# Performance work log

Hardware: AMD Instinct MI355X
Metric: run time of the kernel (lower is better)

## Reference

```python
import jax, jax.numpy as jnp
import numpy as np

SZ = 3072
D = 1024
B, T = 4, 8192
VOCAB = 50257


def setup_inputs() -> dict:
    key = jax.random.key(0)
    k1, k2, k3 = jax.random.split(key, 3)
    t = jax.random.randint(k1, (B, T), 0, VOCAB, dtype=jnp.int32)
    tab = jax.random.normal(k2, (SZ, D), dtype=jnp.float32)
    w_proj = jax.random.normal(k3, (D, D), dtype=jnp.float32) / np.sqrt(D)
    return {"t": t, "tab": tab, "w_proj": w_proj}


def _hash_idx(t, sz):
    # prev token, padded with 0 at position 0
    prev = jnp.pad(t[:, :-1], ((0, 0), (1, 0)))
    # (t*31337 + prev*1000003) % sz, computed overflow-safely in int32
    # using modular arithmetic: (a*b) % m == ((a%m)*(b%m)) % m
    a = (t % sz) * (31337 % sz)
    b = (prev % sz) * (1000003 % sz)
    return (a + b) % sz


def reference(t, tab, w_proj):
    idx = _hash_idx(t, SZ)              # [B, T] in [0, SZ)
    emb = tab[idx]                      # [B, T, D] gather
    # F.linear(x, W) = x @ W.T
    return jnp.einsum('btd,ed->bte', emb, w_proj)
```

## Files before the change

kernel.cpp:

```cpp
#include <hip/hip_runtime.h>
#include <hip/hip_bf16.h>
#include <stdint.h>

#define SZ 3072
#define D_ 1024
#define BB 4
#define TT 8192
#define NROWS (BB * TT)

typedef unsigned short u16;
typedef __bf16 bf16x8 __attribute__((ext_vector_type(8)));
typedef float f32x4 __attribute__((ext_vector_type(4)));


__device__ __forceinline__ u16 f2bf(float f) {
    union { float f; uint32_t u; } c;
    c.f = f;
    uint32_t u = c.u;
    uint32_t r = (u + 0x7FFFu + ((u >> 16) & 1u)) >> 16;
    return (u16)r;
}

__device__ __forceinline__ void gload_lds16(const void* g, void* l) {
    __builtin_amdgcn_global_load_lds(
        (__attribute__((address_space(1))) void*)(void*)g,
        (__attribute__((address_space(3))) void*)l,
        16, 0, 0);
}

__device__ __forceinline__ int hash_pair(int cur, int prev) {
    int a = (cur % SZ) * (31337 % SZ);
    int b = (prev % SZ) * (1000003 % SZ);
    return (a + b) % SZ;
}


__global__ __launch_bounds__(256) void convert_kernel(
    const float* __restrict__ tab, const float* __restrict__ w,
    u16* __restrict__ tabb, u16* __restrict__ wb) {
    const int NT4 = SZ * D_ / 4;
    const int NTOT = NT4 + D_ * D_ / 4;
    int i = blockIdx.x * 256 + threadIdx.x;
    if (i >= NTOT) return;
    const float4* src;
    u16* dst;
    int o;
    if (i < NT4) { src = (const float4*)tab; dst = tabb; o = i; }
    else         { src = (const float4*)w;   dst = wb;   o = i - NT4; }
    float4 v = src[o];
    unsigned long long pack =
        (unsigned long long)f2bf(v.x) |
        ((unsigned long long)f2bf(v.y) << 16) |
        ((unsigned long long)f2bf(v.z) << 32) |
        ((unsigned long long)f2bf(v.w) << 48);
    *(unsigned long long*)&dst[o * 4] = pack;
}


__global__ __launch_bounds__(256) void hash_kernel(
    const int* __restrict__ t, int* __restrict__ idx) {
    int i = blockIdx.x * 256 + threadIdx.x;
    if (i >= NROWS) return;
    int j = i & (TT - 1);
    int cur = t[i];
    int prev = (j == 0) ? 0 : t[i - 1];
    idx[i] = hash_pair(cur, prev);
}


__global__ __launch_bounds__(256) void gemm_p_kernel(
    const u16* __restrict__ Ab,
    const u16* __restrict__ Wb,
    float* __restrict__ P) {
    __shared__ __align__(16) u16 As[128][32];
    __shared__ __align__(16) u16 Ws[128][32];

    const int tid = threadIdx.x;
    const int brow = blockIdx.x >> 3;
    const int bcol = blockIdx.x & 7;
    const int row0 = brow << 7;
    const int col0 = bcol << 7;
    const int lane = tid & 63;
    const int w = tid >> 6;
    const int wr = (w >> 1) << 6;
    const int wc = (w & 1) << 6;
    const int lrow = lane & 15;
    const int k8 = (lane >> 4) << 3;

    const int c0 = tid, c1 = tid + 256;
    const int r0 = c0 >> 2, kk0 = (c0 & 3) << 3;
    const int r1 = c1 >> 2, kk1 = (c1 & 3) << 3;

    f32x4 acc[4][4];
#pragma unroll
    for (int m = 0; m < 4; ++m)
#pragma unroll
        for (int n = 0; n < 4; ++n)
            acc[m][n] = f32x4{0.f, 0.f, 0.f, 0.f};

    for (int k0 = 0; k0 < D_; k0 += 32) {
        gload_lds16(&Ab[(row0 + r0) * D_ + k0 + kk0], &As[r0][kk0]);
        gload_lds16(&Ab[(row0 + r1) * D_ + k0 + kk1], &As[r1][kk1]);
        gload_lds16(&Wb[(col0 + r0) * D_ + k0 + kk0], &Ws[r0][kk0]);
        gload_lds16(&Wb[(col0 + r1) * D_ + k0 + kk1], &Ws[r1][kk1]);
        __syncthreads();

        bf16x8 av[4], bv[4];
#pragma unroll
        for (int m = 0; m < 4; ++m)
            av[m] = *(const bf16x8*)&As[wr + m * 16 + lrow][k8];
#pragma unroll
        for (int n = 0; n < 4; ++n)
            bv[n] = *(const bf16x8*)&Ws[wc + n * 16 + lrow][k8];
#pragma unroll
        for (int m = 0; m < 4; ++m)
#pragma unroll
            for (int n = 0; n < 4; ++n)
                acc[m][n] = __builtin_amdgcn_mfma_f32_16x16x32_bf16(
                    av[m], bv[n], acc[m][n], 0, 0, 0);
        __syncthreads();
    }

    const int rbase = (lane >> 4) << 2;
#pragma unroll
    for (int m = 0; m < 4; ++m)
#pragma unroll
        for (int n = 0; n < 4; ++n)
#pragma unroll
            for (int r = 0; r < 4; ++r)
                P[(row0 + wr + m * 16 + rbase + r) * D_ + col0 + wc + n * 16 + lrow] =
                    acc[m][n][r];
}


__global__ __launch_bounds__(256) void gather_kernel(
    const float* __restrict__ P, const int* __restrict__ idx,
    float* __restrict__ out) {
    const int total = NROWS * (D_ / 4);
    const float4* P4 = (const float4*)P;
    float4* O4 = (float4*)out;
    for (int v = blockIdx.x * 256 + threadIdx.x; v < total; v += gridDim.x * 256) {
        int row = v >> 8;
        int c4 = v & 255;
        int s = idx[row];
        O4[v] = P4[s * 256 + c4];
    }
}


__global__ __launch_bounds__(256) void fallback_kernel(
    const int* __restrict__ t, const float* __restrict__ tab,
    const float* __restrict__ w, float* __restrict__ out) {
    __shared__ float emb[D_];
    int row = blockIdx.x;
    int j = row & (TT - 1);
    int cur = t[row];
    int prev = (j == 0) ? 0 : t[row - 1];
    int s = hash_pair(cur, prev);
    for (int d = threadIdx.x; d < D_; d += 256) emb[d] = tab[s * D_ + d];
    __syncthreads();
    for (int e = threadIdx.x; e < D_; e += 256) {
        float accv = 0.f;
        const float* wrow = &w[e * D_];
        for (int d = 0; d < D_; ++d) accv += emb[d] * wrow[d];
        out[(size_t)row * D_ + e] = accv;
    }
}


extern "C" void kernel_launch(void* const* d_in, const int* in_sizes, int n_in,
                              void* d_out, int out_size, void* d_ws, size_t ws_size,
                              hipStream_t stream) {
    const int* t = (const int*)d_in[0];
    const float* tab = (const float*)d_in[1];
    const float* w = (const float*)d_in[2];
    float* out = (float*)d_out;

    const size_t off_tabb = 0;
    const size_t off_wb   = (size_t)SZ * D_ * 2;
    const size_t off_P    = off_wb + (size_t)D_ * D_ * 2;
    const size_t off_idx  = off_P + (size_t)SZ * D_ * 4;
    const size_t need     = off_idx + (size_t)NROWS * 4;

    if (ws_size < need) {
        fallback_kernel<<<NROWS, 256, 0, stream>>>(t, tab, w, out);
        return;
    }

    u16* tabb = (u16*)((char*)d_ws + off_tabb);
    u16* wb   = (u16*)((char*)d_ws + off_wb);
    float* P  = (float*)((char*)d_ws + off_P);
    int* idx  = (int*)((char*)d_ws + off_idx);

    convert_kernel<<<4096, 256, 0, stream>>>(tab, w, tabb, wb);
    hash_kernel<<<NROWS / 256, 256, 0, stream>>>(t, idx);
    gemm_p_kernel<<<(SZ / 128) * (D_ / 128), 256, 0, stream>>>(tabb, wb, P);
    gather_kernel<<<2048, 256, 0, stream>>>(P, idx, out);
}
```

Before: 194.0 us.

## Fuse hash into gather, shrink GEMM tiles to 64x64 with XCD remap, nontemporal stores

Drops the separate hash kernel and its index buffer by recomputing the hash inside the gather kernel from the token array. The output is written with nontemporal stores so the large streaming output does not pollute cache. The projection GEMM tile shrinks from 128x128 to 64x64, giving four times as many workgroups, and block ids are remapped across the eight XCDs. The smaller tiles raise parallelism on a small GEMM but lower data reuse per workgroup.

```diff
diff --git a/kernel.cpp b/kernel.cpp
--- a/kernel.cpp
+++ b/kernel.cpp
@@ -57,65 +57,53 @@
 }
 
 
-__global__ __launch_bounds__(256) void hash_kernel(
-    const int* __restrict__ t, int* __restrict__ idx) {
-    int i = blockIdx.x * 256 + threadIdx.x;
-    if (i >= NROWS) return;
-    int j = i & (TT - 1);
-    int cur = t[i];
-    int prev = (j == 0) ? 0 : t[i - 1];
-    idx[i] = hash_pair(cur, prev);
-}
-
-
 __global__ __launch_bounds__(256) void gemm_p_kernel(
     const u16* __restrict__ Ab,
     const u16* __restrict__ Wb,
     float* __restrict__ P) {
-    __shared__ __align__(16) u16 As[128][32];
-    __shared__ __align__(16) u16 Ws[128][32];
+    __shared__ __align__(16) u16 As[64][32];
+    __shared__ __align__(16) u16 Ws[64][32];
+
+    const int bid = blockIdx.x;
+    const int wgid = (bid & 7) * 96 + (bid >> 3);
+    const int brow = wgid >> 4;
+    const int bcol = wgid & 15;
+    const int row0 = brow << 6;
+    const int col0 = bcol << 6;
 
     const int tid = threadIdx.x;
-    const int brow = blockIdx.x >> 3;
-    const int bcol = blockIdx.x & 7;
-    const int row0 = brow << 7;
-    const int col0 = bcol << 7;
     const int lane = tid & 63;
     const int w = tid >> 6;
-    const int wr = (w >> 1) << 6;
-    const int wc = (w & 1) << 6;
+    const int wr = (w >> 1) << 5;
+    const int wc = (w & 1) << 5;
     const int lrow = lane & 15;
     const int k8 = (lane >> 4) << 3;
 
-    const int c0 = tid, c1 = tid + 256;
-    const int r0 = c0 >> 2, kk0 = (c0 & 3) << 3;
-    const int r1 = c1 >> 2, kk1 = (c1 & 3) << 3;
+    const int r0 = tid >> 2, kk0 = (tid & 3) << 3;
 
-    f32x4 acc[4][4];
+    f32x4 acc[2][2];
 #pragma unroll
-    for (int m = 0; m < 4; ++m)
+    for (int m = 0; m < 2; ++m)
 #pragma unroll
-        for (int n = 0; n < 4; ++n)
+        for (int n = 0; n < 2; ++n)
             acc[m][n] = f32x4{0.f, 0.f, 0.f, 0.f};
 
     for (int k0 = 0; k0 < D_; k0 += 32) {
         gload_lds16(&Ab[(row0 + r0) * D_ + k0 + kk0], &As[r0][kk0]);
-        gload_lds16(&Ab[(row0 + r1) * D_ + k0 + kk1], &As[r1][kk1]);
         gload_lds16(&Wb[(col0 + r0) * D_ + k0 + kk0], &Ws[r0][kk0]);
-        gload_lds16(&Wb[(col0 + r1) * D_ + k0 + kk1], &Ws[r1][kk1]);
         __syncthreads();
 
-        bf16x8 av[4], bv[4];
+        bf16x8 av[2], bv[2];
 #pragma unroll
-        for (int m = 0; m < 4; ++m)
+        for (int m = 0; m < 2; ++m)
             av[m] = *(const bf16x8*)&As[wr + m * 16 + lrow][k8];
 #pragma unroll
-        for (int n = 0; n < 4; ++n)
+        for (int n = 0; n < 2; ++n)
             bv[n] = *(const bf16x8*)&Ws[wc + n * 16 + lrow][k8];
 #pragma unroll
-        for (int m = 0; m < 4; ++m)
+        for (int m = 0; m < 2; ++m)
 #pragma unroll
-            for (int n = 0; n < 4; ++n)
+            for (int n = 0; n < 2; ++n)
                 acc[m][n] = __builtin_amdgcn_mfma_f32_16x16x32_bf16(
                     av[m], bv[n], acc[m][n], 0, 0, 0);
         __syncthreads();
@@ -123,9 +111,9 @@
 
     const int rbase = (lane >> 4) << 2;
 #pragma unroll
-    for (int m = 0; m < 4; ++m)
+    for (int m = 0; m < 2; ++m)
 #pragma unroll
-        for (int n = 0; n < 4; ++n)
+        for (int n = 0; n < 2; ++n)
 #pragma unroll
             for (int r = 0; r < 4; ++r)
                 P[(row0 + wr + m * 16 + rbase + r) * D_ + col0 + wc + n * 16 + lrow] =
@@ -134,16 +122,19 @@
 
 
 __global__ __launch_bounds__(256) void gather_kernel(
-    const float* __restrict__ P, const int* __restrict__ idx,
+    const float* __restrict__ P, const int* __restrict__ t,
     float* __restrict__ out) {
     const int total = NROWS * (D_ / 4);
-    const float4* P4 = (const float4*)P;
-    float4* O4 = (float4*)out;
+    const f32x4* P4 = (const f32x4*)P;
+    f32x4* O4 = (f32x4*)out;
     for (int v = blockIdx.x * 256 + threadIdx.x; v < total; v += gridDim.x * 256) {
         int row = v >> 8;
         int c4 = v & 255;
-        int s = idx[row];
-        O4[v] = P4[s * 256 + c4];
+        int cur = t[row];
+        int prev = ((row & (TT - 1)) == 0) ? 0 : t[row - 1];
+        int s = hash_pair(cur, prev);
+        f32x4 val = P4[s * 256 + c4];
+        __builtin_nontemporal_store(val, &O4[v]);
     }
 }
 
@@ -179,8 +170,7 @@
     const size_t off_tabb = 0;
     const size_t off_wb   = (size_t)SZ * D_ * 2;
     const size_t off_P    = off_wb + (size_t)D_ * D_ * 2;
-    const size_t off_idx  = off_P + (size_t)SZ * D_ * 4;
-    const size_t need     = off_idx + (size_t)NROWS * 4;
+    const size_t need     = off_P + (size_t)SZ * D_ * 4;
 
     if (ws_size < need) {
         fallback_kernel<<<NROWS, 256, 0, stream>>>(t, tab, w, out);
@@ -190,10 +180,8 @@
     u16* tabb = (u16*)((char*)d_ws + off_tabb);
     u16* wb   = (u16*)((char*)d_ws + off_wb);
     float* P  = (float*)((char*)d_ws + off_P);
-    int* idx  = (int*)((char*)d_ws + off_idx);
 
     convert_kernel<<<4096, 256, 0, stream>>>(tab, w, tabb, wb);
-    hash_kernel<<<NROWS / 256, 256, 0, stream>>>(t, idx);
-    gemm_p_kernel<<<(SZ / 128) * (D_ / 128), 256, 0, stream>>>(tabb, wb, P);
-    gather_kernel<<<2048, 256, 0, stream>>>(P, idx, out);
+    gemm_p_kernel<<<(SZ / 64) * (D_ / 64), 256, 0, stream>>>(tabb, wb, P);
+    gather_kernel<<<2048, 256, 0, stream>>>(P, t, out);
 }
```

New measurement: 188.9 us. 1.03x faster.
